# Performance work log

Measured on AMD Instinct MI355X. Metric: run time of the kernel, lower is better.

Reference implementation:

```python
import jax, jax.numpy as jnp
import numpy as np

D_MODEL = 1024
NUM_HEADS = 16
HEAD_DIM = D_MODEL // NUM_HEADS
B, S = 4, 2048


def setup_inputs() -> dict:
    key = jax.random.key(0)
    ks = jax.random.split(key, 11)
    scale = 1.0 / np.sqrt(D_MODEL)
    return {
        "query": jax.random.normal(ks[0], (B, S, D_MODEL), jnp.float32),
        "key": jax.random.normal(ks[1], (B, S, D_MODEL), jnp.float32),
        "value": jax.random.normal(ks[2], (B, S, D_MODEL), jnp.float32),
        "Wq": jax.random.normal(ks[3], (D_MODEL, D_MODEL), jnp.float32) * scale,
        "bq": jnp.zeros((D_MODEL,), jnp.float32),
        "Wk": jax.random.normal(ks[4], (D_MODEL, D_MODEL), jnp.float32) * scale,
        "bk": jnp.zeros((D_MODEL,), jnp.float32),
        "Wv": jax.random.normal(ks[5], (D_MODEL, D_MODEL), jnp.float32) * scale,
        "bv": jnp.zeros((D_MODEL,), jnp.float32),
        "Wo": jax.random.normal(ks[6], (D_MODEL, D_MODEL), jnp.float32) * scale,
        "bo": jnp.zeros((D_MODEL,), jnp.float32),
    }


def reference(query, key, value, Wq, bq, Wk, bk, Wv, bv, Wo, bo):
    b = query.shape[0]
    # nn.Linear: x @ W.T + b; weights stored [out, in]
    def split_heads(x):
        return x.reshape(b, -1, NUM_HEADS, HEAD_DIM).transpose(0, 2, 1, 3)  # [b,h,s,d]
    q = split_heads(query @ Wq.T + bq)
    k = split_heads(key @ Wk.T + bk)
    v = split_heads(value @ Wv.T + bv)
    scores = jnp.einsum("bhqd,bhkd->bhqk", q, k) / np.sqrt(HEAD_DIM)
    weights = jax.nn.softmax(scores, axis=-1)
    out = jnp.einsum("bhqk,bhkd->bhqd", weights, v)
    out = out.transpose(0, 2, 1, 3).reshape(b, -1, D_MODEL)
    return out @ Wo.T + bo
```

## Files before the change

kernel.cpp:

```cpp
#include <hip/hip_runtime.h>

typedef __bf16 bf16;
typedef __bf16 bf16x4 __attribute__((ext_vector_type(4)));
typedef __bf16 bf16x8 __attribute__((ext_vector_type(8)));
typedef float f32x4 __attribute__((ext_vector_type(4)));

#define MFMA16(a, b, c) __builtin_amdgcn_mfma_f32_16x16x32_bf16((a), (b), (c), 0, 0, 0)

#define QSCALE 0.1803368808f

__device__ __forceinline__ void async_cp16(const bf16* g, bf16* l) {
    __builtin_amdgcn_global_load_lds((const __attribute__((address_space(1))) void*)g,
                                     (__attribute__((address_space(3))) void*)l, 16, 0, 0);
}

struct CvtArgs { const float* src[7]; bf16* dst[7]; };
__global__ void cvt_all(CvtArgs a) {
    int bx = blockIdx.x, t, off;
    if (bx < 12288) { t = bx >> 12;            off = bx & 4095; }
    else            { t = 3 + ((bx - 12288) >> 9); off = (bx - 12288) & 511; }
    size_t i = (size_t)off * 256 + threadIdx.x;
    const float4* p = (const float4*)(a.src[t] + i * 8);
    float4 x = p[0], y = p[1];
    bf16x8 o;
    o[0] = (bf16)x.x; o[1] = (bf16)x.y; o[2] = (bf16)x.z; o[3] = (bf16)x.w;
    o[4] = (bf16)y.x; o[5] = (bf16)y.y; o[6] = (bf16)y.z; o[7] = (bf16)y.w;
    *(bf16x8*)(a.dst[t] + i * 8) = o;
}

__device__ __forceinline__ void gemm_core(
    const bf16* __restrict__ A, const bf16* __restrict__ W,
    const float* __restrict__ bias, void* __restrict__ Cout,
    int mode, int m0, int n0)
{
    __shared__ bf16 As[128 * 64];
    __shared__ bf16 Bs[128 * 64];
    const int K = 1024;
    const int tid = threadIdx.x;
    const int lane = tid & 63, wave = tid >> 6;
    const int l15 = lane & 15, quad = lane >> 4, l7 = l15 & 7;
    const int wm = wave >> 1, wn = wave & 1;

    f32x4 acc[4][4] = {};

    const int rb = tid >> 3;
    const int cg8 = ((tid & 7) ^ (rb & 7)) * 8;
    const bf16* Ag = A + (size_t)(m0 + rb) * K + cg8;
    const bf16* Wg = W + (size_t)(n0 + rb) * K + cg8;
    bf16* Al = As + tid * 8;
    bf16* Bl = Bs + tid * 8;

    for (int k0 = 0; k0 < K; k0 += 64) {
        __syncthreads();
#pragma unroll
        for (int j = 0; j < 4; ++j) {
            async_cp16(Ag + k0 + (size_t)(j * 32) * K, Al + j * 2048);
            async_cp16(Wg + k0 + (size_t)(j * 32) * K, Bl + j * 2048);
        }
        __syncthreads();

#pragma unroll
        for (int ks = 0; ks < 2; ++ks) {
            bf16x8 af[4], bfr[4];
#pragma unroll
            for (int t = 0; t < 4; ++t) {
                const int sw = ((ks * 4 + quad) ^ l7) * 8;
                af[t]  = *(const bf16x8*)(As + (wm * 64 + t * 16 + l15) * 64 + sw);
                bfr[t] = *(const bf16x8*)(Bs + (wn * 64 + t * 16 + l15) * 64 + sw);
            }
#pragma unroll
            for (int mt = 0; mt < 4; ++mt)
#pragma unroll
                for (int nt = 0; nt < 4; ++nt)
                    acc[mt][nt] = MFMA16(af[mt], bfr[nt], acc[mt][nt]);
        }
    }

#pragma unroll
    for (int mt = 0; mt < 4; ++mt) {
#pragma unroll
        for (int nt = 0; nt < 4; ++nt) {
            int col = n0 + wn * 64 + nt * 16 + l15;
            float bcol = (mode == 2) ? 0.0f : bias[col];
#pragma unroll
            for (int r = 0; r < 4; ++r) {
                int row = m0 + wm * 64 + mt * 16 + quad * 4 + r;
                float val = acc[mt][nt][r];
                if (mode == 2) {
                    val += bias[row];
                    int bb = col >> 11, s = col & 2047;
                    int u = s & 31;
                    int sp = (s & ~31) | (((u >> 2) & 3) * 8 + (u >> 4) * 4 + (u & 3));
                    ((bf16*)Cout)[((size_t)(bb * 1024 + row) << 11) + sp] = (bf16)val;
                } else if (mode == 3) {
                    ((float*)Cout)[(size_t)row * 1024 + col] = val + bcol;
                } else {
                    val += bcol;
                    if (mode == 0) val *= QSCALE;
                    int bb = row >> 11, s = row & 2047, hh = col >> 6, d = col & 63;
                    ((bf16*)Cout)[(((size_t)(bb * 16 + hh) * 2048 + s) << 6) + d] = (bf16)val;
                }
            }
        }
    }
}

struct QkvArgs {
    const bf16* A[3];
    const bf16* W[3];
    const float* bias[3];
    bf16* out[3];
};

__global__ __launch_bounds__(256) void qkv_gemm(QkvArgs t) {
    int z = blockIdx.y;
    int bid = blockIdx.x;
    int lo = bid & 7, mid = (bid >> 3) & 7, hi = bid >> 6;
    int m0, n0;
    if (z < 2) { m0 = (lo + hi * 8) * 128; n0 = mid * 128; }
    else       { m0 = mid * 128;           n0 = (lo + hi * 8) * 128; }
    gemm_core(t.A[z], t.W[z], t.bias[z], t.out[z], z, m0, n0);
}

__global__ __launch_bounds__(256) void oproj_gemm(
    const bf16* __restrict__ A, const bf16* __restrict__ W,
    const float* __restrict__ bias, float* __restrict__ Cout) {
    gemm_core(A, W, bias, Cout, 3, blockIdx.x * 128, blockIdx.y * 128);
}

__global__ __launch_bounds__(256, 2) void attn_kernel(
    const bf16* __restrict__ Qh, const bf16* __restrict__ Kh,
    const bf16* __restrict__ Vtg, bf16* __restrict__ AO)
{
    __shared__ bf16 Kl[64 * 64];
    __shared__ bf16 Vl[64 * 64];

    const int tid = threadIdx.x;
    const int lane = tid & 63, wave = tid >> 6;
    const int l15 = lane & 15, quad = lane >> 4, l7 = l15 & 7;
    const int g = blockIdx.x & 63, qi = blockIdx.x >> 6;
    const int h = g & 15, b = g >> 4;
    const size_t base = (size_t)(b * 16 + h) << 17;
    const int q0 = qi * 256 + wave * 64;

    bf16x8 qf[4][2];
#pragma unroll
    for (int qt = 0; qt < 4; ++qt)
#pragma unroll
        for (int ks = 0; ks < 2; ++ks)
            qf[qt][ks] = *(const bf16x8*)(Qh + base + (q0 + qt * 16 + l15) * 64 + ks * 32 + quad * 8);

    f32x4 o[4][4] = {};
    float ls[4] = {};

    const int sr = tid >> 3;
    const int sc0 = ((tid & 7) ^ (sr & 7)) * 8;
    const int sr2 = sr + 32;

    for (int kt = 0; kt < 2048; kt += 64) {
        __syncthreads();
        async_cp16(Kh + base + (size_t)(kt + sr) * 64 + sc0, Kl + tid * 8);
        async_cp16(Kh + base + (size_t)(kt + sr2) * 64 + sc0, Kl + (tid + 256) * 8);
        async_cp16(Vtg + base + (size_t)sr * 2048 + kt + sc0, Vl + tid * 8);
        async_cp16(Vtg + base + (size_t)sr2 * 2048 + kt + sc0, Vl + (tid + 256) * 8);
        __syncthreads();

        bf16x8 kb[2][4];
#pragma unroll
        for (int ks = 0; ks < 2; ++ks)
#pragma unroll
            for (int ktile = 0; ktile < 4; ++ktile)
                kb[ks][ktile] = *(const bf16x8*)(Kl + (ktile * 16 + l15) * 64 + (((ks * 4 + quad) ^ l7) * 8));

        bf16x8 pf[4][2];
#pragma unroll
        for (int qt = 0; qt < 4; ++qt) {
            f32x4 sc[4] = {};
#pragma unroll
            for (int ks = 0; ks < 2; ++ks)
#pragma unroll
                for (int ktile = 0; ktile < 4; ++ktile)
                    sc[ktile] = MFMA16(kb[ks][ktile], qf[qt][ks], sc[ktile]);
            float sum = 0.0f;
#pragma unroll
            for (int kc = 0; kc < 2; ++kc) {
                bf16x8 pk;
#pragma unroll
                for (int t = 0; t < 2; ++t)
#pragma unroll
                    for (int r = 0; r < 4; ++r) {
                        float p = __builtin_amdgcn_exp2f(sc[kc * 2 + t][r]);
                        sum += p;
                        pk[t * 4 + r] = (bf16)p;
                    }
                pf[qt][kc] = pk;
            }
            ls[qt] += sum;
        }

        bf16x8 va[4][2];
#pragma unroll
        for (int dt = 0; dt < 4; ++dt)
#pragma unroll
            for (int kc = 0; kc < 2; ++kc)
                va[dt][kc] = *(const bf16x8*)(Vl + (dt * 16 + l15) * 64 + (((kc * 4 + quad) ^ l7) * 8));

#pragma unroll
        for (int dt = 0; dt < 4; ++dt)
#pragma unroll
            for (int qt = 0; qt < 4; ++qt)
#pragma unroll
                for (int kc = 0; kc < 2; ++kc)
                    o[dt][qt] = MFMA16(va[dt][kc], pf[qt][kc], o[dt][qt]);
    }

#pragma unroll
    for (int qt = 0; qt < 4; ++qt) {
        float l = ls[qt];
        l += __shfl_xor(l, 16, 64);
        l += __shfl_xor(l, 32, 64);
        float inv = 1.0f / l;
        size_t rb = ((size_t)(b * 2048 + q0 + qt * 16 + l15)) * 1024 + h * 64;
#pragma unroll
        for (int dt = 0; dt < 4; ++dt) {
            bf16x4 ov = {(bf16)(o[dt][qt][0] * inv), (bf16)(o[dt][qt][1] * inv),
                         (bf16)(o[dt][qt][2] * inv), (bf16)(o[dt][qt][3] * inv)};
            *(bf16x4*)(AO + rb + dt * 16 + quad * 4) = ov;
        }
    }
}

extern "C" void kernel_launch(void* const* d_in, const int* in_sizes, int n_in,
                              void* d_out, int out_size, void* d_ws, size_t ws_size,
                              hipStream_t stream) {
    const float* q  = (const float*)d_in[0];
    const float* k  = (const float*)d_in[1];
    const float* v  = (const float*)d_in[2];
    const float* Wq = (const float*)d_in[3];
    const float* bq = (const float*)d_in[4];
    const float* Wk = (const float*)d_in[5];
    const float* bk = (const float*)d_in[6];
    const float* Wv = (const float*)d_in[7];
    const float* bv = (const float*)d_in[8];
    const float* Wo = (const float*)d_in[9];
    const float* bo = (const float*)d_in[10];
    float* out = (float*)d_out;

    const size_t NX = (size_t)8192 * 1024;
    const size_t NW = (size_t)1024 * 1024;
    bf16* ws  = (bf16*)d_ws;
    bf16* Xq  = ws;
    bf16* Xk  = Xq + NX;
    bf16* Xv  = Xk + NX;
    bf16* Wqb = Xv + NX;
    bf16* Wkb = Wqb + NW;
    bf16* Wvb = Wkb + NW;
    bf16* Wob = Wvb + NW;
    bf16* Qh  = Wob + NW;
    bf16* Kh  = Qh + NX;
    bf16* Vt  = Kh + NX;
    bf16* AO  = Xq;

    CvtArgs ca;
    ca.src[0] = q;  ca.dst[0] = Xq;
    ca.src[1] = k;  ca.dst[1] = Xk;
    ca.src[2] = v;  ca.dst[2] = Xv;
    ca.src[3] = Wq; ca.dst[3] = Wqb;
    ca.src[4] = Wk; ca.dst[4] = Wkb;
    ca.src[5] = Wv; ca.dst[5] = Wvb;
    ca.src[6] = Wo; ca.dst[6] = Wob;
    cvt_all<<<14336, 256, 0, stream>>>(ca);

    QkvArgs t;
    t.A[0] = Xq;  t.W[0] = Wqb; t.bias[0] = bq; t.out[0] = Qh;
    t.A[1] = Xk;  t.W[1] = Wkb; t.bias[1] = bk; t.out[1] = Kh;
    t.A[2] = Wvb; t.W[2] = Xv;  t.bias[2] = bv; t.out[2] = Vt;
    qkv_gemm<<<dim3(512, 3), dim3(256, 1, 1), 0, stream>>>(t);

    attn_kernel<<<512, 256, 0, stream>>>(Qh, Kh, Vt, AO);

    oproj_gemm<<<dim3(64, 8), dim3(256, 1, 1), 0, stream>>>(AO, Wob, bo, out);
}
```

Before: 337.6 us.

## Double-buffer LDS tiles in GEMM and attention kernels to overlap loads with MFMA

Both the projection GEMM and the attention kernel now use two LDS buffers per operand. The next K/V or A/W tile is issued with async global-to-LDS copies before the MFMA work on the current tile, and a single vmcnt wait plus barrier closes each step. This hides global memory latency behind compute and halves the barriers per iteration. In exchange it doubles LDS use (64KB in the GEMM, 32KB in attention), which may reduce occupancy, especially for the attention kernel that requests 2 blocks per CU.

After: 370.9 us. 9.9% more time.

```diff
diff --git a/kernel.cpp b/kernel.cpp
--- a/kernel.cpp
+++ b/kernel.cpp
@@ -33,8 +33,8 @@
     const float* __restrict__ bias, void* __restrict__ Cout,
     int mode, int m0, int n0)
 {
-    __shared__ bf16 As[128 * 64];
-    __shared__ bf16 Bs[128 * 64];
+    __shared__ bf16 As0[128 * 64], As1[128 * 64];
+    __shared__ bf16 Bs0[128 * 64], Bs1[128 * 64];
     const int K = 1024;
     const int tid = threadIdx.x;
     const int lane = tid & 63, wave = tid >> 6;
@@ -47,26 +47,26 @@
     const int cg8 = ((tid & 7) ^ (rb & 7)) * 8;
     const bf16* Ag = A + (size_t)(m0 + rb) * K + cg8;
     const bf16* Wg = W + (size_t)(n0 + rb) * K + cg8;
-    bf16* Al = As + tid * 8;
-    bf16* Bl = Bs + tid * 8;
-
-    for (int k0 = 0; k0 < K; k0 += 64) {
-        __syncthreads();
+
+    auto stageTo = [&](bf16* Al, bf16* Bl, int k0) {
 #pragma unroll
         for (int j = 0; j < 4; ++j) {
-            async_cp16(Ag + k0 + (size_t)(j * 32) * K, Al + j * 2048);
-            async_cp16(Wg + k0 + (size_t)(j * 32) * K, Bl + j * 2048);
-        }
-        __syncthreads();
-
+            async_cp16(Ag + k0 + (size_t)(j * 32) * K, Al + tid * 8 + j * 2048);
+            async_cp16(Wg + k0 + (size_t)(j * 32) * K, Bl + tid * 8 + j * 2048);
+        }
+    };
+
+    auto step = [&](const bf16* Ac, const bf16* Bc, bf16* An, bf16* Bn,
+                    int kn, bool doStage) {
+        if (doStage) stageTo(An, Bn, kn);
 #pragma unroll
         for (int ks = 0; ks < 2; ++ks) {
             bf16x8 af[4], bfr[4];
 #pragma unroll
             for (int t = 0; t < 4; ++t) {
                 const int sw = ((ks * 4 + quad) ^ l7) * 8;
-                af[t]  = *(const bf16x8*)(As + (wm * 64 + t * 16 + l15) * 64 + sw);
-                bfr[t] = *(const bf16x8*)(Bs + (wn * 64 + t * 16 + l15) * 64 + sw);
+                af[t]  = *(const bf16x8*)(Ac + (wm * 64 + t * 16 + l15) * 64 + sw);
+                bfr[t] = *(const bf16x8*)(Bc + (wn * 64 + t * 16 + l15) * 64 + sw);
             }
 #pragma unroll
             for (int mt = 0; mt < 4; ++mt)
@@ -74,7 +74,20 @@
                 for (int nt = 0; nt < 4; ++nt)
                     acc[mt][nt] = MFMA16(af[mt], bfr[nt], acc[mt][nt]);
         }
+        asm volatile("s_waitcnt vmcnt(0)" ::: "memory");
+        __builtin_amdgcn_s_barrier();
+    };
+
+    stageTo(As0, Bs0, 0);
+    asm volatile("s_waitcnt vmcnt(0)" ::: "memory");
+    __builtin_amdgcn_s_barrier();
+
+    for (int p = 0; p < 7; ++p) {
+        step(As0, Bs0, As1, Bs1, p * 128 + 64, true);
+        step(As1, Bs1, As0, Bs0, p * 128 + 128, true);
     }
+    step(As0, Bs0, As1, Bs1, 960, true);
+    step(As1, Bs1, As0, Bs0, 0, false);
 
 #pragma unroll
     for (int mt = 0; mt < 4; ++mt) {
@@ -132,8 +145,8 @@
     const bf16* __restrict__ Qh, const bf16* __restrict__ Kh,
     const bf16* __restrict__ Vtg, bf16* __restrict__ AO)
 {
-    __shared__ bf16 Kl[64 * 64];
-    __shared__ bf16 Vl[64 * 64];
+    __shared__ bf16 Kl0[64 * 64], Kl1[64 * 64];
+    __shared__ bf16 Vl0[64 * 64], Vl1[64 * 64];
 
     const int tid = threadIdx.x;
     const int lane = tid & 63, wave = tid >> 6;
@@ -157,20 +170,23 @@
     const int sc0 = ((tid & 7) ^ (sr & 7)) * 8;
     const int sr2 = sr + 32;
 
-    for (int kt = 0; kt < 2048; kt += 64) {
-        __syncthreads();
-        async_cp16(Kh + base + (size_t)(kt + sr) * 64 + sc0, Kl + tid * 8);
-        async_cp16(Kh + base + (size_t)(kt + sr2) * 64 + sc0, Kl + (tid + 256) * 8);
-        async_cp16(Vtg + base + (size_t)sr * 2048 + kt + sc0, Vl + tid * 8);
-        async_cp16(Vtg + base + (size_t)sr2 * 2048 + kt + sc0, Vl + (tid + 256) * 8);
-        __syncthreads();
+    auto stageTo = [&](bf16* Kn, bf16* Vn, int kt) {
+        async_cp16(Kh + base + (size_t)(kt + sr) * 64 + sc0, Kn + tid * 8);
+        async_cp16(Kh + base + (size_t)(kt + sr2) * 64 + sc0, Kn + (tid + 256) * 8);
+        async_cp16(Vtg + base + (size_t)sr * 2048 + kt + sc0, Vn + tid * 8);
+        async_cp16(Vtg + base + (size_t)sr2 * 2048 + kt + sc0, Vn + (tid + 256) * 8);
+    };
+
+    auto step = [&](const bf16* Kc, const bf16* Vc, bf16* Kn, bf16* Vn,
+                    int ktn, bool doStage) {
+        if (doStage) stageTo(Kn, Vn, ktn);
 
         bf16x8 kb[2][4];
 #pragma unroll
         for (int ks = 0; ks < 2; ++ks)
 #pragma unroll
             for (int ktile = 0; ktile < 4; ++ktile)
-                kb[ks][ktile] = *(const bf16x8*)(Kl + (ktile * 16 + l15) * 64 + (((ks * 4 + quad) ^ l7) * 8));
+                kb[ks][ktile] = *(const bf16x8*)(Kc + (ktile * 16 + l15) * 64 + (((ks * 4 + quad) ^ l7) * 8));
 
         bf16x8 pf[4][2];
 #pragma unroll
@@ -203,7 +219,7 @@
         for (int dt = 0; dt < 4; ++dt)
 #pragma unroll
             for (int kc = 0; kc < 2; ++kc)
-                va[dt][kc] = *(const bf16x8*)(Vl + (dt * 16 + l15) * 64 + (((kc * 4 + quad) ^ l7) * 8));
+                va[dt][kc] = *(const bf16x8*)(Vc + (dt * 16 + l15) * 64 + (((kc * 4 + quad) ^ l7) * 8));
 
 #pragma unroll
         for (int dt = 0; dt < 4; ++dt)
@@ -212,7 +228,21 @@
 #pragma unroll
                 for (int kc = 0; kc < 2; ++kc)
                     o[dt][qt] = MFMA16(va[dt][kc], pf[qt][kc], o[dt][qt]);
+
+        asm volatile("s_waitcnt vmcnt(0)" ::: "memory");
+        __builtin_amdgcn_s_barrier();
+    };
+
+    stageTo(Kl0, Vl0, 0);
+    asm volatile("s_waitcnt vmcnt(0)" ::: "memory");
+    __builtin_amdgcn_s_barrier();
+
+    for (int p = 0; p < 15; ++p) {
+        step(Kl0, Vl0, Kl1, Vl1, p * 128 + 64, true);
+        step(Kl1, Vl1, Kl0, Vl0, p * 128 + 128, true);
     }
+    step(Kl0, Vl0, Kl1, Vl1, 1984, true);
+    step(Kl1, Vl1, Kl0, Vl0, 0, false);
 
 #pragma unroll
     for (int qt = 0; qt < 4; ++qt) {
```
